# Kernel optimization log

Hardware: AMD Instinct MI355X
Metric: run time of the kernel (lower is better)

Reference implementation:

```python
import jax, jax.numpy as jnp
import numpy as np

NEG = -1e9


def _ln(x, g, b):
    m = x.mean(-1, keepdims=True)
    v = ((x - m) ** 2).mean(-1, keepdims=True)
    return (x - m) / jnp.sqrt(v + 1e-5) * g + b


def _block(single, pair, single_mask, pair_mask,
           pa_ln_g, pa_ln_b, pa_wqkv, pa_wg, pa_wout,
           pt_ln_g, pt_ln_b, pt_w1, pt_b1, pt_w2, pt_b2,
           sa_ln_g, sa_ln_b, sa_wq, sa_wkv, sa_wb, sa_wout,
           st_ln_g, st_ln_b, st_w1, st_b1, st_w2, st_b2):
    B, L, _, D = pair.shape
    H = sa_wb.shape[1]
    hd = D // H
    scale = 1.0 / jnp.sqrt(jnp.asarray(hd, dtype=pair.dtype))
    # ---- PairUpdate: PairAttention over L*L pseudo-tokens ----
    z = _ln(pair, pa_ln_g, pa_ln_b)                       # [B,L,L,D]
    N = L * L
    qkv = (z @ pa_wqkv).reshape(B, N, 3, H, hd)
    q = qkv[:, :, 0].transpose(0, 2, 1, 3)                # [B,H,N,hd]
    k = qkv[:, :, 1].transpose(0, 2, 1, 3)
    v = qkv[:, :, 2].transpose(0, 2, 1, 3)
    attn = jnp.einsum('bhid,bhjd->bhij', q, k) * scale    # [B,H,N,N]
    pm = pair_mask.reshape(B, 1, N)
    m = pm[:, :, :, None] * pm[:, :, None, :]             # [B,1,N,N]
    attn = jnp.where(m > 0, attn, NEG)
    attn = jax.nn.softmax(attn, axis=-1)
    out = jnp.einsum('bhij,bhjd->bhid', attn, v)          # [B,H,N,hd]
    out = out.transpose(0, 2, 1, 3).reshape(B, L, L, D)
    g = jax.nn.sigmoid(z @ pa_wg)
    out = (out @ pa_wout) * g * pair_mask[..., None]
    pair = pair + out
    t = _ln(pair, pt_ln_g, pt_ln_b)
    t = jax.nn.relu(t @ pt_w1 + pt_b1) @ pt_w2 + pt_b2
    pair = pair + t * pair_mask[..., None]
    # ---- SingleUpdate: AttentionPairBias ----
    s = _ln(single, sa_ln_g, sa_ln_b)                     # [B,L,D]
    q = (s @ sa_wq).reshape(B, L, H, hd)
    kv = (s @ sa_wkv).reshape(B, L, 2, H, hd)
    k2, v2 = kv[:, :, 0], kv[:, :, 1]
    attn = jnp.einsum('bihd,bjhd->bhij', q, k2) * scale   # [B,H,L,L]
    bias = (pair @ sa_wb).transpose(0, 3, 1, 2)           # [B,H,L,L]
    attn = attn + bias
    sm = single_mask[:, None, None, :]
    attn = jnp.where(sm > 0, attn, NEG)
    attn = jax.nn.softmax(attn, axis=-1)
    out = jnp.einsum('bhij,bjhd->bihd', attn, v2).reshape(B, L, D)
    single = single + (out @ sa_wout) * single_mask[..., None]
    # single transition
    t = _ln(single, st_ln_g, st_ln_b)
    t = jax.nn.relu(t @ st_w1 + st_b1) @ st_w2 + st_b2
    single = single + t * single_mask[..., None]
    return single, pair


def setup_inputs() -> dict:
    key = jax.random.key(0)
    B, L, D, H = 1, 64, 144, 8
    ks = iter(jax.random.split(key, 40))
    def nrm(shape, scale=0.02):
        return jax.random.normal(next(ks), shape, dtype=jnp.float32) * scale
    sm = jnp.ones((B, L), jnp.float32).at[:, L - 8:].set(0.0)
    pm = sm[:, :, None] * sm[:, None, :]
    return dict(
        single=jax.random.normal(next(ks), (B, L, D), jnp.float32),
        pair=jax.random.normal(next(ks), (B, L, L, D), jnp.float32),
        single_mask=sm,
        pair_mask=pm,
        pa_ln_g=jnp.ones((D,), jnp.float32), pa_ln_b=jnp.zeros((D,), jnp.float32),
        pa_wqkv=nrm((D, 3 * D)), pa_wg=nrm((D, D)), pa_wout=nrm((D, D)),
        pt_ln_g=jnp.ones((D,), jnp.float32), pt_ln_b=jnp.zeros((D,), jnp.float32),
        pt_w1=nrm((D, 4 * D)), pt_b1=jnp.zeros((4 * D,), jnp.float32),
        pt_w2=nrm((4 * D, D)), pt_b2=jnp.zeros((D,), jnp.float32),
        sa_ln_g=jnp.ones((D,), jnp.float32), sa_ln_b=jnp.zeros((D,), jnp.float32),
        sa_wq=nrm((D, D)), sa_wkv=nrm((D, 2 * D)), sa_wb=nrm((D, H)), sa_wout=nrm((D, D)),
        st_ln_g=jnp.ones((D,), jnp.float32), st_ln_b=jnp.zeros((D,), jnp.float32),
        st_w1=nrm((D, 4 * D)), st_b1=jnp.zeros((4 * D,), jnp.float32),
        st_w2=nrm((4 * D, D)), st_b2=jnp.zeros((D,), jnp.float32),
    )


def reference(single, pair, single_mask, pair_mask,
              pa_ln_g, pa_ln_b, pa_wqkv, pa_wg, pa_wout,
              pt_ln_g, pt_ln_b, pt_w1, pt_b1, pt_w2, pt_b2,
              sa_ln_g, sa_ln_b, sa_wq, sa_wkv, sa_wb, sa_wout,
              st_ln_g, st_ln_b, st_w1, st_b1, st_w2, st_b2):
    return _block(single, pair, single_mask, pair_mask,
                  pa_ln_g, pa_ln_b, pa_wqkv, pa_wg, pa_wout,
                  pt_ln_g, pt_ln_b, pt_w1, pt_b1, pt_w2, pt_b2,
                  sa_ln_g, sa_ln_b, sa_wq, sa_wkv, sa_wb, sa_wout,
                  st_ln_g, st_ln_b, st_w1, st_b1, st_w2, st_b2)
```

## Files before the change

kernel.cpp:

```cpp
#include <hip/hip_runtime.h>
#include <hip/hip_bf16.h>

typedef __hip_bfloat16 bf16;
typedef __attribute__((ext_vector_type(8))) short short8;
typedef __attribute__((ext_vector_type(16))) float floatx16;
typedef __attribute__((ext_vector_type(4))) unsigned int uint4v;

__device__ __forceinline__ float tof(bf16 x){ return __bfloat162float(x); }
__device__ __forceinline__ float bflo(unsigned u){ return __uint_as_float(u<<16); }
__device__ __forceinline__ float bfhi(unsigned u){ return __uint_as_float(u & 0xFFFF0000u); }
__device__ __forceinline__ float ldT(const void* p, long i, bool isf){
  return isf ? ((const float*)p)[i] : tof(((const bf16*)p)[i]);
}
__device__ __forceinline__ void stT(void* p, long i, bool isf, float v){
  if (isf) ((float*)p)[i] = v; else ((bf16*)p)[i] = __float2bfloat16(v);
}

#define LL 64
#define DD 144
#define NN 4096
#define HH 8
#define HDIM 18
#define SCALE 0.23570226039551584f
#define LOG2E 1.4426950408889634f

__global__ __launch_bounds__(256) void prep_weights(const unsigned* __restrict__ smaskw,
    int* __restrict__ dflag,
    const void* __restrict__ wqkv, const void* __restrict__ wg,
    const void* __restrict__ wout, const void* __restrict__ w1, const void* __restrict__ w2,
    const void* __restrict__ swq, const void* __restrict__ swkv,
    const void* __restrict__ swout, const void* __restrict__ sw1, const void* __restrict__ sw2,
    bf16* __restrict__ F1, bf16* __restrict__ Fout, bf16* __restrict__ Fw1,
    bf16* __restrict__ Fw2, bf16* __restrict__ Fs1, bf16* __restrict__ Wtswout,
    bf16* __restrict__ Wtst1, bf16* __restrict__ Wtst2){
  bool isf = (smaskw[0] == 0x3F800000u);
  if (blockIdx.x==0 && threadIdx.x==0) dflag[0] = isf ? 4 : 2;
  long t = (long)blockIdx.x*256 + threadIdx.x;
  if (t < 82944){
    int j=t&7, lane=(int)((t>>3)&63); long tk=t>>9; int ks=tk%9, tile=tk/9;
    int col=tile*32+(lane&31); int k=ks*16+(lane>>5)*8+j;
    float v = (col<432)? ldT(wqkv,(long)k*432+col,isf) : ldT(wg,(long)k*144+(col-432),isf);
    F1[t]=__float2bfloat16(v); return;
  } t -= 82944;
  if (t < 23040){
    int j=t&7, lane=(int)((t>>3)&63); long tk=t>>9; int ks=tk%9, tile=tk/9;
    int col=tile*32+(lane&31); if (col>143) col=143;
    int k=ks*16+(lane>>5)*8+j;
    Fout[t]=__float2bfloat16(ldT(wout,(long)k*144+col,isf)); return;
  } t -= 23040;
  if (t < 82944){
    int j=t&7, lane=(int)((t>>3)&63); long tk=t>>9; int ks=tk%9, tile=tk/9;
    int col=tile*32+(lane&31); int k=ks*16+(lane>>5)*8+j;
    Fw1[t]=__float2bfloat16(ldT(w1,(long)k*576+col,isf)); return;
  } t -= 82944;
  if (t < 92160){
    int j=t&7, lane=(int)((t>>3)&63); long tk=t>>9; int ks=tk%36, tile=tk/36;
    int col=tile*32+(lane&31); if (col>143) col=143;
    int k=ks*16+(lane>>5)*8+j;
    Fw2[t]=__float2bfloat16(ldT(w2,(long)k*144+col,isf)); return;
  } t -= 92160;
  if (t < 64512){
    int j=t&7, lane=(int)((t>>3)&63); long tk=t>>9; int ks=tk%9, tile=tk/9;
    int col=tile*32+(lane&31); if (col>431) col=431;
    int k=ks*16+(lane>>5)*8+j;
    float v = (col<144)? ldT(swq,(long)k*144+col,isf) : ldT(swkv,(long)k*288+(col-144),isf);
    Fs1[t]=__float2bfloat16(v); return;
  } t -= 64512;
  if (t < 20736){ int c=t/144,k=t-(long)c*144; Wtswout[t]=__float2bfloat16(ldT(swout,(long)k*144+c,isf)); return; }
  t -= 20736;
  if (t < 82944){ int c=t/144,k=t-(long)c*144; Wtst1[t]=__float2bfloat16(ldT(sw1,(long)k*576+c,isf)); return; }
  t -= 82944;
  if (t < 82944){ int c=t/576,k=t-(long)c*576; Wtst2[t]=__float2bfloat16(ldT(sw2,(long)k*144+c,isf)); return; }
}

__global__ __launch_bounds__(256) void gemm_fused1(const int* __restrict__ df,
    const void* __restrict__ pairv, const void* __restrict__ lng, const void* __restrict__ lnb,
    const bf16* __restrict__ F1,
    const void* __restrict__ pmask,
    bf16* __restrict__ Qb, bf16* __restrict__ Kf, bf16* __restrict__ Vf,
    bf16* __restrict__ gbuf,
    const void* __restrict__ singlev, const void* __restrict__ sag, const void* __restrict__ sab,
    const bf16* __restrict__ Fs1,
    bf16* __restrict__ q_sb, bf16* __restrict__ kv_sb){
  __shared__ short As[64*152];
  bool isf = df[0]==4;
  int tid=threadIdx.x, lane=tid&63, l31=lane&31, w=tid>>6, wr=w>>1, wc=w&1;
  int g=(lane>>5)*8;

  if (blockIdx.y == 64){
    if (blockIdx.x >= 7) return;
    for (int rr=w; rr<64; rr+=4){
      long base=(long)rr*DD;
      float e0=ldT(singlev,base+lane,isf), e1=ldT(singlev,base+lane+64,isf);
      float e2=(lane<16)?ldT(singlev,base+lane+128,isf):0.f;
      float s=e0+e1+e2;
      #pragma unroll
      for (int o=32;o;o>>=1) s += __shfl_xor(s,o);
      float mean=s*(1.f/144.f);
      float d0=e0-mean, d1=e1-mean, d2=(lane<16)?(e2-mean):0.f;
      float v=d0*d0+d1*d1+d2*d2;
      #pragma unroll
      for (int o=32;o;o>>=1) v += __shfl_xor(v,o);
      float rstd=rsqrtf(v*(1.f/144.f)+1e-5f);
      bf16 h0=__float2bfloat16(d0*rstd*ldT(sag,lane,isf)+ldT(sab,lane,isf));
      bf16 h1=__float2bfloat16(d1*rstd*ldT(sag,lane+64,isf)+ldT(sab,lane+64,isf));
      As[rr*152+lane]=*reinterpret_cast<short*>(&h0);
      As[rr*152+lane+64]=*reinterpret_cast<short*>(&h1);
      if (lane<16){
        bf16 h2=__float2bfloat16(d2*rstd*ldT(sag,lane+128,isf)+ldT(sab,lane+128,isf));
        As[rr*152+lane+128]=*reinterpret_cast<short*>(&h2);
      }
    }
    __syncthreads();
    int tile = blockIdx.x*2 + wc;
    const short8* wf = (const short8*)Fs1;
    floatx16 acc;
    #pragma unroll
    for (int i=0;i<16;i++) acc[i]=0.f;
    #pragma unroll
    for (int ks=0; ks<9; ks++){
      short8 af = *(const short8*)&As[(l31+32*wr)*152 + ks*16 + g];
      acc = __builtin_amdgcn_mfma_f32_32x32x16_bf16(af, wf[(tile*9+ks)*64+lane], acc, 0,0,0);
    }
    int col = tile*32 + l31;
    if (col < 432){
      #pragma unroll
      for (int r=0;r<16;r++){
        int row = 32*wr + (r&3)+8*(r>>2)+4*(lane>>5);
        if (col<144) q_sb[(size_t)row*DD+col] = __float2bfloat16(acc[r]);
        else kv_sb[(size_t)row*288+(col-144)] = __float2bfloat16(acc[r]);
      }
    }
    return;
  }

  int row0 = blockIdx.y*64, col0 = blockIdx.x*64;
  for (int rr=w; rr<64; rr+=4){
    long base=(long)(row0+rr)*DD;
    float e0=ldT(pairv,base+lane,isf), e1=ldT(pairv,base+lane+64,isf);
    float e2=(lane<16)?ldT(pairv,base+lane+128,isf):0.f;
    float s=e0+e1+e2;
    #pragma unroll
    for (int o=32;o;o>>=1) s += __shfl_xor(s,o);
    float mean=s*(1.f/144.f);
    float d0=e0-mean, d1=e1-mean, d2=(lane<16)?(e2-mean):0.f;
    float v=d0*d0+d1*d1+d2*d2;
    #pragma unroll
    for (int o=32;o;o>>=1) v += __shfl_xor(v,o);
    float rstd=rsqrtf(v*(1.f/144.f)+1e-5f);
    bf16 h0=__float2bfloat16(d0*rstd*ldT(lng,lane,isf)+ldT(lnb,lane,isf));
    bf16 h1=__float2bfloat16(d1*rstd*ldT(lng,lane+64,isf)+ldT(lnb,lane+64,isf));
    As[rr*152+lane]=*reinterpret_cast<short*>(&h0);
    As[rr*152+lane+64]=*reinterpret_cast<short*>(&h1);
    if (lane<16){
      bf16 h2=__float2bfloat16(d2*rstd*ldT(lng,lane+128,isf)+ldT(lnb,lane+128,isf));
      As[rr*152+lane+128]=*reinterpret_cast<short*>(&h2);
    }
  }
  __syncthreads();
  int tile = blockIdx.x*2 + wc;
  const short8* wf = (const short8*)F1;
  floatx16 acc;
  #pragma unroll
  for (int i=0;i<16;i++) acc[i]=0.f;
  #pragma unroll
  for (int ks=0; ks<9; ks++){
    short8 af = *(const short8*)&As[(l31+32*wr)*152 + ks*16 + g];
    acc = __builtin_amdgcn_mfma_f32_32x32x16_bf16(af, wf[(tile*9+ks)*64+lane], acc, 0,0,0);
  }
  int col = col0 + wc*32 + l31;
  #pragma unroll
  for (int r=0;r<16;r++){
    int row = row0 + 32*wr + (r&3)+8*(r>>2)+4*(lane>>5);
    if (col < 144){
      int hh = col/18, d = col - hh*18;
      Qb[((size_t)hh*NN+row)*32 + d] = __float2bfloat16(acc[r]*(SCALE*LOG2E));
    } else if (col < 288){
      int c2 = col-144, hh = c2/18, d = c2 - hh*18;
      int f = d>>4, rem = d&15, gs = rem>>3, j = rem&7;
      Kf[((((size_t)hh*128 + (row>>5))*2 + f)*64 + gs*32 + (row&31))*8 + j]
        = __float2bfloat16(acc[r]);
    } else if (col < 432){
      int c2 = col-288, hh = c2/18, d = c2 - hh*18;
      float pm = (ldT(pmask,row,isf)>0.f)?1.f:0.f;
      int kin = row&31, f = kin>>4, k15 = kin&15;
      int gs = (k15>>2)&1, j = (k15&3) | (((k15>>3)&1)<<2);
      Vf[((((size_t)hh*128 + (row>>5))*2 + f)*64 + gs*32 + d)*8 + j]
        = __float2bfloat16(acc[r]*pm);
    } else {
      int c2 = col-432;
      float gt = 1.f/(1.f+__expf(fminf(-acc[r],30.f)));
      gbuf[(size_t)row*DD+c2] = __float2bfloat16(gt);
    }
  }
  if (blockIdx.x==0){
    for (int t=threadIdx.x; t<64*8*7; t+=256){
      int n = row0 + t/56; int rem = t%56; int hh = rem/7, dw = rem%7 + 9;
      ((unsigned*)(Qb + ((size_t)hh*NN+n)*32))[dw] = 0;
    }
    for (int t=threadIdx.x; t<64*8; t+=256){
      int n = row0 + (t>>3), hh = t&7;
      float pm = (ldT(pmask,n,isf)>0.f)?1.f:0.f;
      int kin = n&31, f = kin>>4, k15 = kin&15;
      int gs = (k15>>2)&1, j = (k15&3) | (((k15>>3)&1)<<2);
      Vf[((((size_t)hh*128 + (n>>5))*2 + f)*64 + gs*32 + 18)*8 + j] = __float2bfloat16(pm);
    }
  }
}

__global__ __launch_bounds__(256) void pair_attn_mfma(const int* __restrict__ df,
    const bf16* __restrict__ Qb, const bf16* __restrict__ Kf,
    const bf16* __restrict__ Vf, bf16* __restrict__ aob){
  __shared__ float Comb[4][32][20];
  int h = blockIdx.x & 7, qt = blockIdx.x >> 3;
  int tid = threadIdx.x;
  int w = tid >> 6, lane = tid & 63;
  int l31 = lane & 31, gsel = lane>>5;

  const unsigned* qp = (const unsigned*)(Qb + ((size_t)h*NN + qt*32 + l31)*32);
  short8 qf0, qf1;
  #pragma unroll
  for (int j=0;j<4;j++) ((unsigned*)&qf0)[j] = qp[gsel*4+j];
  #pragma unroll
  for (int j=0;j<4;j++) ((unsigned*)&qf1)[j] = qp[8+gsel*4+j];

  floatx16 o;
  #pragma unroll
  for (int i=0;i<16;i++) o[i]=0.f;

  const short8* kf8 = (const short8*)Kf + (size_t)h*16384;
  const short8* vf8 = (const short8*)Vf + (size_t)h*16384;
  int c0 = w*32;

  short8 af0 = kf8[(c0*2+0)*64 + lane];
  short8 af1 = kf8[(c0*2+1)*64 + lane];
  short8 av0 = vf8[(c0*2+0)*64 + lane];
  short8 av1 = vf8[(c0*2+1)*64 + lane];

  for (int cc=0; cc<32; cc++){
    int cn = c0 + (cc<31 ? cc+1 : 31);
    short8 naf0 = kf8[(cn*2+0)*64 + lane];
    short8 naf1 = kf8[(cn*2+1)*64 + lane];
    short8 nav0 = vf8[(cn*2+0)*64 + lane];
    short8 nav1 = vf8[(cn*2+1)*64 + lane];

    floatx16 s;
    #pragma unroll
    for (int i=0;i<16;i++) s[i]=0.f;
    __builtin_amdgcn_s_setprio(1);
    s = __builtin_amdgcn_mfma_f32_32x32x16_bf16(af0, qf0, s, 0,0,0);
    s = __builtin_amdgcn_mfma_f32_32x32x16_bf16(af1, qf1, s, 0,0,0);
    __builtin_amdgcn_s_setprio(0);

    short8 P1, P2;
    #pragma unroll
    for (int j=0;j<4;j++){
      unsigned e0 = __float_as_uint(__builtin_amdgcn_exp2f(s[2*j]));
      unsigned e1 = __float_as_uint(__builtin_amdgcn_exp2f(s[2*j+1]));
      ((unsigned*)&P1)[j] = (e0>>16) | (e1 & 0xFFFF0000u);
      unsigned e2 = __float_as_uint(__builtin_amdgcn_exp2f(s[8+2*j]));
      unsigned e3 = __float_as_uint(__builtin_amdgcn_exp2f(s[9+2*j]));
      ((unsigned*)&P2)[j] = (e2>>16) | (e3 & 0xFFFF0000u);
    }

    __builtin_amdgcn_s_setprio(1);
    o = __builtin_amdgcn_mfma_f32_32x32x16_bf16(av0, P1, o, 0,0,0);
    o = __builtin_amdgcn_mfma_f32_32x32x16_bf16(av1, P2, o, 0,0,0);
    __builtin_amdgcn_s_setprio(0);

    af0=naf0; af1=naf1; av0=nav0; av1=nav1;
  }

  #pragma unroll
  for (int r=0;r<16;r++){
    int d = (r&3) + 8*(r>>2) + 4*gsel;
    if (d < 20) Comb[w][l31][d] = o[r];
  }
  __syncthreads();
  for (int t=tid; t<32*HDIM; t+=256){
    int q = t/HDIM, d = t-q*HDIM;
    float num = Comb[0][q][d]+Comb[1][q][d]+Comb[2][q][d]+Comb[3][q][d];
    float den = Comb[0][q][18]+Comb[1][q][18]+Comb[2][q][18]+Comb[3][q][18];
    aob[(size_t)(qt*32+q)*DD + h*HDIM + d] = __float2bfloat16(num/fmaxf(den,1e-20f));
  }
}

__global__ __launch_bounds__(512) void pair_tail(const int* __restrict__ df,
    const bf16* __restrict__ aob, const bf16* __restrict__ gbuf,
    const void* __restrict__ pairv, const void* __restrict__ pmaskv,
    const bf16* __restrict__ Fout, const void* __restrict__ ptln_g, const void* __restrict__ ptln_b,
    const bf16* __restrict__ Fw1, const void* __restrict__ b1v,
    const bf16* __restrict__ Fw2, const void* __restrict__ b2v,
    const void* __restrict__ wb, void* __restrict__ outP, long outOff,
    float* __restrict__ biasb){
  __shared__ __align__(16) char smem[65536];
  float* p1  = (float*)smem;
  short* ts  = (short*)(smem + 18432);
  short* hh_ = (short*)(smem + 28160);
  float* outv = (float*)(smem + 28160);

  bool isf = df[0]==4;
  int tid=threadIdx.x, lane=tid&63, l31=lane&31, gsel=lane>>5, g=gsel*8;
  int w=tid>>6;
  int r0 = blockIdx.x*32;
  const short8* foutf = (const short8*)Fout;
  const short8* fw1f  = (const short8*)Fw1;
  const short8* fw2f  = (const short8*)Fw2;

  for (int t=tid; t<32*72; t+=512){
    int m=t/72, dw=t%72;
    ((unsigned*)ts)[m*76+dw] = ((const unsigned*)(aob + (size_t)(r0+m)*144))[dw];
  }
  __syncthreads();

  for (int tile=w; tile<5; tile+=8){
    int c0=tile*32;
    floatx16 acc;
    #pragma unroll
    for (int i=0;i<16;i++) acc[i]=0.f;
    #pragma unroll
    for (int ks=0; ks<9; ks++){
      short8 af = *(const short8*)&ts[l31*152 + ks*16 + g];
      acc = __builtin_amdgcn_mfma_f32_32x32x16_bf16(af, foutf[(tile*9+ks)*64+lane], acc, 0,0,0);
    }
    if (c0+l31 < 144){
      #pragma unroll
      for (int r=0;r<16;r++){
        int row=(r&3)+8*(r>>2)+4*gsel;
        p1[row*144 + c0+l31] = acc[r];
      }
    }
  }
  __syncthreads();
  for (int t=tid; t<32*144; t+=512){
    int row=t/144; int col=t-row*144;
    long gidx=(long)(r0+row)*144 + col;
    float pm = (ldT(pmaskv, r0+row, isf)>0.f)?1.f:0.f;
    p1[t] = ldT(pairv,gidx,isf) + p1[t]*tof(gbuf[gidx])*pm;
  }
  __syncthreads();
  for (int rr=w; rr<32; rr+=8){
    float e0=p1[rr*144+lane], e1=p1[rr*144+lane+64], e2=(lane<16)?p1[rr*144+lane+128]:0.f;
    float s=e0+e1+e2;
    #pragma unroll
    for (int o=32;o;o>>=1) s += __shfl_xor(s,o);
    float mean=s*(1.f/144.f);
    float d0=e0-mean, d1=e1-mean, d2=(lane<16)?(e2-mean):0.f;
    float v=d0*d0+d1*d1+d2*d2;
    #pragma unroll
    for (int o=32;o;o>>=1) v += __shfl_xor(v,o);
    float rstd=rsqrtf(v*(1.f/144.f)+1e-5f);
    bf16 h0 = __float2bfloat16(d0*rstd*ldT(ptln_g,lane,isf)    + ldT(ptln_b,lane,isf));
    bf16 h1 = __float2bfloat16(d1*rstd*ldT(ptln_g,lane+64,isf) + ldT(ptln_b,lane+64,isf));
    ts[rr*152+lane]    = *reinterpret_cast<short*>(&h0);
    ts[rr*152+lane+64] = *reinterpret_cast<short*>(&h1);
    if (lane<16){
      bf16 h2 = __float2bfloat16(d2*rstd*ldT(ptln_g,lane+128,isf) + ldT(ptln_b,lane+128,isf));
      ts[rr*152+lane+128] = *reinterpret_cast<short*>(&h2);
    }
  }
  __syncthreads();
  for (int tile=w; tile<18; tile+=8){
    int c0=tile*32, colB=c0+l31;
    floatx16 acc;
    #pragma unroll
    for (int i=0;i<16;i++) acc[i]=0.f;
    #pragma unroll
    for (int ks=0; ks<9; ks++){
      short8 af = *(const short8*)&ts[l31*152 + ks*16 + g];
      acc = __builtin_amdgcn_mfma_f32_32x32x16_bf16(af, fw1f[(tile*9+ks)*64+lane], acc, 0,0,0);
    }
    float bb = ldT(b1v,colB,isf);
    #pragma unroll
    for (int r=0;r<16;r++){
      int row=(r&3)+8*(r>>2)+4*gsel;
      bf16 hv = __float2bfloat16(fmaxf(acc[r]+bb,0.f));
      hh_[row*584 + colB] = *reinterpret_cast<short*>(&hv);
    }
  }
  __syncthreads();
  floatx16 fin; int fc0 = -1;
  for (int tile=w; tile<5; tile+=8){
    int c0=tile*32;
    int colB=c0+l31; if (colB>143) colB=143;
    floatx16 acc;
    #pragma unroll
    for (int i=0;i<16;i++) acc[i]=0.f;
    #pragma unroll
    for (int ks=0; ks<36; ks++){
      short8 af = *(const short8*)&hh_[l31*584 + ks*16 + g];
      acc = __builtin_amdgcn_mfma_f32_32x32x16_bf16(af, fw2f[(tile*36+ks)*64+lane], acc, 0,0,0);
    }
    float bb = ldT(b2v,colB,isf);
    #pragma unroll
    for (int r=0;r<16;r++){
      int row=(r&3)+8*(r>>2)+4*gsel;
      float pm = (ldT(pmaskv, r0+row, isf)>0.f)?1.f:0.f;
      float val = p1[row*144 + colB] + (acc[r]+bb)*pm;
      if (c0+l31 < 144)
        stT(outP, outOff + (long)(r0+row)*144 + c0+l31, isf, val);
      fin[r]=val;
    }
    fc0 = c0;
  }
  __syncthreads();
  if (fc0 >= 0 && fc0+l31 < 144){
    #pragma unroll
    for (int r=0;r<16;r++){
      int row=(r&3)+8*(r>>2)+4*gsel;
      outv[row*144 + fc0+l31] = fin[r];
    }
  }
  __syncthreads();
  if (tid < 256){
    int n = tid>>3, hb = tid&7;
    float acc=0.f;
    #pragma unroll 4
    for (int k=0;k<144;k++) acc += outv[n*144+k]*ldT(wb,k*8+hb,isf);
    biasb[(size_t)(r0+n)*8+hb]=acc;
  }
}

__global__ __launch_bounds__(256) void single_tail(const int* __restrict__ df,
    const void* __restrict__ single, const bf16* __restrict__ q_sb,
    const bf16* __restrict__ kv_sb, const float* __restrict__ biasb,
    const void* __restrict__ smask, const bf16* __restrict__ Wtswout,
    const void* __restrict__ stln_g, const void* __restrict__ stln_b,
    const bf16* __restrict__ Wtst1, const void* __restrict__ st_b1,
    const bf16* __restrict__ Wtst2, const void* __restrict__ st_b2,
    void* __restrict__ outS){
  bool isf = df[0]==4;
  __shared__ __align__(16) short kvs[64*288];
  __shared__ float pexp[8][64];
  __shared__ float tot[8];
  __shared__ __align__(16) float bb[512];
  __shared__ float qs[DD], as_[DD], s1[DD], tss[DD], hs[576];
  __shared__ float mr[2];
  int n = blockIdx.x, tid = threadIdx.x;
  {
    const uint4v* src = (const uint4v*)kv_sb;
    uint4v* dst = (uint4v*)kvs;
    for (int t=tid; t<2304; t+=256) dst[t] = src[t];
  }
  if (tid<DD) qs[tid] = tof(q_sb[(size_t)n*DD+tid]);
  {
    const uint4v* src = (const uint4v*)(biasb + (size_t)n*512);
    uint4v* dst = (uint4v*)bb;
    if (tid<128) dst[tid] = src[tid];
  }
  __syncthreads();
  #pragma unroll
  for (int pp=0; pp<2; pp++){
    int pi = tid + pp*256;
    int h = pi>>6, j = pi&63;
    const unsigned* kr = (const unsigned*)&kvs[j*288 + h*HDIM];
    float s=0.f;
    #pragma unroll
    for (int i=0;i<9;i++){
      unsigned u = kr[i];
      s += qs[h*HDIM+2*i]*bflo(u) + qs[h*HDIM+2*i+1]*bfhi(u);
    }
    s = fminf(s*SCALE + bb[j*8+h], 30.f);
    pexp[h][j] = (ldT(smask,j,isf)>0.f) ? __expf(s) : 0.f;
  }
  __syncthreads();
  if (tid<64){
    int h=tid>>3, j0=(tid&7)*8;
    float t2=0.f;
    #pragma unroll
    for (int j=0;j<8;j++) t2 += pexp[h][j0+j];
    #pragma unroll
    for (int o=4;o;o>>=1) t2 += __shfl_xor(t2,o);
    if ((tid&7)==0) tot[h] = fmaxf(t2,1e-20f);
  }
  __syncthreads();
  if (tid<DD){
    int h = tid/HDIM;
    float a0=0.f, a1=0.f;
    #pragma unroll 8
    for (int j=0;j<64;j+=2){
      unsigned u0 = ((unsigned)(unsigned short)kvs[j*288 + 144 + tid])<<16;
      unsigned u1 = ((unsigned)(unsigned short)kvs[(j+1)*288 + 144 + tid])<<16;
      a0 += pexp[h][j]*__uint_as_float(u0);
      a1 += pexp[h][j+1]*__uint_as_float(u1);
    }
    as_[tid] = (a0+a1)/tot[h];
  }
  __syncthreads();
  float sm = ldT(smask,n,isf);
  if (tid<DD){
    const uint4v* wr = (const uint4v*)(Wtswout + (size_t)tid*DD);
    float a0=0.f, a1=0.f;
    #pragma unroll 3
    for (int kw=0; kw<18; kw+=2){
      uint4v u = wr[kw], u2 = wr[kw+1];
      a0 += as_[8*kw+0]*bflo(u[0]) + as_[8*kw+1]*bfhi(u[0])
          + as_[8*kw+2]*bflo(u[1]) + as_[8*kw+3]*bfhi(u[1])
          + as_[8*kw+4]*bflo(u[2]) + as_[8*kw+5]*bfhi(u[2])
          + as_[8*kw+6]*bflo(u[3]) + as_[8*kw+7]*bfhi(u[3]);
      a1 += as_[8*kw+8]*bflo(u2[0]) + as_[8*kw+9]*bfhi(u2[0])
          + as_[8*kw+10]*bflo(u2[1]) + as_[8*kw+11]*bfhi(u2[1])
          + as_[8*kw+12]*bflo(u2[2]) + as_[8*kw+13]*bfhi(u2[2])
          + as_[8*kw+14]*bflo(u2[3]) + as_[8*kw+15]*bfhi(u2[3]);
    }
    s1[tid] = ldT(single,(long)n*DD+tid,isf) + (a0+a1)*sm;
  }
  __syncthreads();
  if (tid < 64){
    float e0 = s1[tid], e1 = s1[tid+64], e2 = (tid<16)?s1[tid+128]:0.f;
    float s = e0+e1+e2;
    #pragma unroll
    for (int o=32;o;o>>=1) s += __shfl_xor(s,o);
    float mean = s*(1.f/144.f);
    float d0=e0-mean, d1=e1-mean, d2=(tid<16)?(e2-mean):0.f;
    float v = d0*d0+d1*d1+d2*d2;
    #pragma unroll
    for (int o=32;o;o>>=1) v += __shfl_xor(v,o);
    if (tid==0){ mr[0]=mean; mr[1]=rsqrtf(v*(1.f/144.f)+1e-5f); }
  }
  __syncthreads();
  if (tid<DD) tss[tid] = (s1[tid]-mr[0])*mr[1]*ldT(stln_g,tid,isf) + ldT(stln_b,tid,isf);
  __syncthreads();
  for (int c=tid;c<576;c+=256){
    const uint4v* wr = (const uint4v*)(Wtst1 + (size_t)c*DD);
    float a0=ldT(st_b1,c,isf), a1=0.f;
    #pragma unroll 3
    for (int kw=0; kw<18; kw+=2){
      uint4v u = wr[kw], u2 = wr[kw+1];
      a0 += tss[8*kw+0]*bflo(u[0]) + tss[8*kw+1]*bfhi(u[0])
          + tss[8*kw+2]*bflo(u[1]) + tss[8*kw+3]*bfhi(u[1])
          + tss[8*kw+4]*bflo(u[2]) + tss[8*kw+5]*bfhi(u[2])
          + tss[8*kw+6]*bflo(u[3]) + tss[8*kw+7]*bfhi(u[3]);
      a1 += tss[8*kw+8]*bflo(u2[0]) + tss[8*kw+9]*bfhi(u2[0])
          + tss[8*kw+10]*bflo(u2[1]) + tss[8*kw+11]*bfhi(u2[1])
          + tss[8*kw+12]*bflo(u2[2]) + tss[8*kw+13]*bfhi(u2[2])
          + tss[8*kw+14]*bflo(u2[3]) + tss[8*kw+15]*bfhi(u2[3]);
    }
    hs[c]=fmaxf(a0+a1,0.f);
  }
  __syncthreads();
  if (tid<DD){
    const uint4v* wr = (const uint4v*)(Wtst2 + (size_t)tid*576);
    float a0=ldT(st_b2,tid,isf), a1=0.f;
    #pragma unroll 4
    for (int kw=0; kw<72; kw+=2){
      uint4v u = wr[kw], u2 = wr[kw+1];
      a0 += hs[8*kw+0]*bflo(u[0]) + hs[8*kw+1]*bfhi(u[0])
          + hs[8*kw+2]*bflo(u[1]) + hs[8*kw+3]*bfhi(u[1])
          + hs[8*kw+4]*bflo(u[2]) + hs[8*kw+5]*bfhi(u[2])
          + hs[8*kw+6]*bflo(u[3]) + hs[8*kw+7]*bfhi(u[3]);
      a1 += hs[8*kw+8]*bflo(u2[0]) + hs[8*kw+9]*bfhi(u2[0])
          + hs[8*kw+10]*bflo(u2[1]) + hs[8*kw+11]*bfhi(u2[1])
          + hs[8*kw+12]*bflo(u2[2]) + hs[8*kw+13]*bfhi(u2[2])
          + hs[8*kw+14]*bflo(u2[3]) + hs[8*kw+15]*bfhi(u2[3]);
    }
    stT(outS,(long)n*DD+tid,isf, s1[tid] + (a0+a1)*sm);
  }
}

extern "C" void kernel_launch(void* const* d_in, const int* in_sizes, int n_in,
                              void* d_out, int out_size, void* d_ws, size_t ws_size,
                              hipStream_t stream) {
  char* wsb = (char*)d_ws;
  int*   dflag = (int*)wsb;
  bf16*  F1     = (bf16*)(wsb + 16);
  bf16*  Fout   = F1 + 82944;
  bf16*  Fw1    = Fout + 23040;
  bf16*  Fw2    = Fw1 + 82944;
  bf16*  Fs1    = Fw2 + 92160;
  bf16*  Wtswout= Fs1 + 64512;
  bf16*  Wtst1  = Wtswout + 20736;
  bf16*  Wtst2  = Wtst1 + 82944;
  bf16*  Qb   = Wtst2 + 82944;
  bf16*  Kf   = Qb + (size_t)HH*NN*32;
  bf16*  Vf   = Kf + (size_t)HH*131072;
  bf16*  gbuf = Vf + (size_t)HH*131072;
  bf16*  aob  = gbuf + (size_t)NN*DD;
  float* biasb= (float*)(aob + (size_t)NN*DD);
  bf16*  q_sb = (bf16*)(biasb + NN*8);
  bf16*  kv_sb= q_sb + LL*DD;

  const long OUTP_OFF = (long)LL*DD;

  prep_weights<<<2079,256,0,stream>>>((const unsigned*)d_in[2], dflag,
      d_in[6], d_in[7], d_in[8], d_in[11], d_in[13],
      d_in[17], d_in[18], d_in[20], d_in[23], d_in[25],
      F1, Fout, Fw1, Fw2, Fs1, Wtswout, Wtst1, Wtst2);

  gemm_fused1<<<dim3(9,65),256,0,stream>>>(dflag, d_in[1], d_in[4], d_in[5], F1, d_in[3],
                                           Qb, Kf, Vf, gbuf,
                                           d_in[0], d_in[15], d_in[16], Fs1, q_sb, kv_sb);
  pair_attn_mfma<<<1024,256,0,stream>>>(dflag, Qb, Kf, Vf, aob);
  pair_tail<<<128,512,0,stream>>>(dflag, aob, gbuf, d_in[1], d_in[3],
                                  Fout, d_in[9], d_in[10], Fw1, d_in[12],
                                  Fw2, d_in[14], d_in[19], d_out, OUTP_OFF, biasb);
  single_tail<<<LL,256,0,stream>>>(dflag, d_in[0], q_sb, kv_sb, biasb, d_in[2],
                                   Wtswout, d_in[21], d_in[22], Wtst1, d_in[24],
                                   Wtst2, d_in[26], d_out);
  (void)in_sizes; (void)n_in; (void)out_size; (void)ws_size;
}
```

Baseline: 225.2 us.

## Process two query tiles per attention block and split single_tail reductions across 512 threads

The pair attention kernel now computes two 32-row query tiles per block. Each loaded K/V fragment is reused for both, which halves K/V global traffic per query, and the grid drops from 1024 to 512 blocks. The cost is more registers for the second accumulator and Q fragments, plus fewer blocks to fill the GPU. Separately, single_tail moves to 512 threads and splits its attention-value, output-projection and FFN2 dot products into segments, reduced through a shared partial buffer, to shorten the serial per-thread loops at the price of extra barriers.

```diff
diff --git a/kernel.cpp b/kernel.cpp
--- a/kernel.cpp
+++ b/kernel.cpp
@@ -212,21 +212,26 @@
     const bf16* __restrict__ Qb, const bf16* __restrict__ Kf,
     const bf16* __restrict__ Vf, bf16* __restrict__ aob){
   __shared__ float Comb[4][32][20];
-  int h = blockIdx.x & 7, qt = blockIdx.x >> 3;
+  int h = blockIdx.x & 7, qp2 = blockIdx.x >> 3;
+  int qtA = qp2*2, qtB = qp2*2+1;
   int tid = threadIdx.x;
   int w = tid >> 6, lane = tid & 63;
   int l31 = lane & 31, gsel = lane>>5;
 
-  const unsigned* qp = (const unsigned*)(Qb + ((size_t)h*NN + qt*32 + l31)*32);
-  short8 qf0, qf1;
+  const unsigned* qpA = (const unsigned*)(Qb + ((size_t)h*NN + qtA*32 + l31)*32);
+  const unsigned* qpB = (const unsigned*)(Qb + ((size_t)h*NN + qtB*32 + l31)*32);
+  short8 qa0, qa1, qb0, qb1;
   #pragma unroll
-  for (int j=0;j<4;j++) ((unsigned*)&qf0)[j] = qp[gsel*4+j];
+  for (int j=0;j<4;j++){
+    ((unsigned*)&qa0)[j] = qpA[gsel*4+j];
+    ((unsigned*)&qa1)[j] = qpA[8+gsel*4+j];
+    ((unsigned*)&qb0)[j] = qpB[gsel*4+j];
+    ((unsigned*)&qb1)[j] = qpB[8+gsel*4+j];
+  }
+
+  floatx16 oA, oB;
   #pragma unroll
-  for (int j=0;j<4;j++) ((unsigned*)&qf1)[j] = qp[8+gsel*4+j];
-
-  floatx16 o;
-  #pragma unroll
-  for (int i=0;i<16;i++) o[i]=0.f;
+  for (int i=0;i<16;i++){ oA[i]=0.f; oB[i]=0.f; }
 
   const short8* kf8 = (const short8*)Kf + (size_t)h*16384;
   const short8* vf8 = (const short8*)Vf + (size_t)h*16384;
@@ -245,14 +250,13 @@
     short8 nav1 = vf8[(cn*2+1)*64 + lane];
 
     floatx16 s;
+    short8 P1, P2;
     #pragma unroll
     for (int i=0;i<16;i++) s[i]=0.f;
     __builtin_amdgcn_s_setprio(1);
-    s = __builtin_amdgcn_mfma_f32_32x32x16_bf16(af0, qf0, s, 0,0,0);
-    s = __builtin_amdgcn_mfma_f32_32x32x16_bf16(af1, qf1, s, 0,0,0);
+    s = __builtin_amdgcn_mfma_f32_32x32x16_bf16(af0, qa0, s, 0,0,0);
+    s = __builtin_amdgcn_mfma_f32_32x32x16_bf16(af1, qa1, s, 0,0,0);
     __builtin_amdgcn_s_setprio(0);
-
-    short8 P1, P2;
     #pragma unroll
     for (int j=0;j<4;j++){
       unsigned e0 = __float_as_uint(__builtin_amdgcn_exp2f(s[2*j]));
@@ -262,10 +266,28 @@
       unsigned e3 = __float_as_uint(__builtin_amdgcn_exp2f(s[9+2*j]));
       ((unsigned*)&P2)[j] = (e2>>16) | (e3 & 0xFFFF0000u);
     }
-
     __builtin_amdgcn_s_setprio(1);
-    o = __builtin_amdgcn_mfma_f32_32x32x16_bf16(av0, P1, o, 0,0,0);
-    o = __builtin_amdgcn_mfma_f32_32x32x16_bf16(av1, P2, o, 0,0,0);
+    oA = __builtin_amdgcn_mfma_f32_32x32x16_bf16(av0, P1, oA, 0,0,0);
+    oA = __builtin_amdgcn_mfma_f32_32x32x16_bf16(av1, P2, oA, 0,0,0);
+    __builtin_amdgcn_s_setprio(0);
+    #pragma unroll
+    for (int i=0;i<16;i++) s[i]=0.f;
+    __builtin_amdgcn_s_setprio(1);
+    s = __builtin_amdgcn_mfma_f32_32x32x16_bf16(af0, qb0, s, 0,0,0);
+    s = __builtin_amdgcn_mfma_f32_32x32x16_bf16(af1, qb1, s, 0,0,0);
+    __builtin_amdgcn_s_setprio(0);
+    #pragma unroll
+    for (int j=0;j<4;j++){
+      unsigned e0 = __float_as_uint(__builtin_amdgcn_exp2f(s[2*j]));
+      unsigned e1 = __float_as_uint(__builtin_amdgcn_exp2f(s[2*j+1]));
+      ((unsigned*)&P1)[j] = (e0>>16) | (e1 & 0xFFFF0000u);
+      unsigned e2 = __float_as_uint(__builtin_amdgcn_exp2f(s[8+2*j]));
+      unsigned e3 = __float_as_uint(__builtin_amdgcn_exp2f(s[9+2*j]));
+      ((unsigned*)&P2)[j] = (e2>>16) | (e3 & 0xFFFF0000u);
+    }
+    __builtin_amdgcn_s_setprio(1);
+    oB = __builtin_amdgcn_mfma_f32_32x32x16_bf16(av0, P1, oB, 0,0,0);
+    oB = __builtin_amdgcn_mfma_f32_32x32x16_bf16(av1, P2, oB, 0,0,0);
     __builtin_amdgcn_s_setprio(0);
 
     af0=naf0; af1=naf1; av0=nav0; av1=nav1;
@@ -274,14 +296,27 @@
   #pragma unroll
   for (int r=0;r<16;r++){
     int d = (r&3) + 8*(r>>2) + 4*gsel;
-    if (d < 20) Comb[w][l31][d] = o[r];
+    if (d < 20) Comb[w][l31][d] = oA[r];
   }
   __syncthreads();
   for (int t=tid; t<32*HDIM; t+=256){
     int q = t/HDIM, d = t-q*HDIM;
     float num = Comb[0][q][d]+Comb[1][q][d]+Comb[2][q][d]+Comb[3][q][d];
     float den = Comb[0][q][18]+Comb[1][q][18]+Comb[2][q][18]+Comb[3][q][18];
-    aob[(size_t)(qt*32+q)*DD + h*HDIM + d] = __float2bfloat16(num/fmaxf(den,1e-20f));
+    aob[(size_t)(qtA*32+q)*DD + h*HDIM + d] = __float2bfloat16(num/fmaxf(den,1e-20f));
+  }
+  __syncthreads();
+  #pragma unroll
+  for (int r=0;r<16;r++){
+    int d = (r&3) + 8*(r>>2) + 4*gsel;
+    if (d < 20) Comb[w][l31][d] = oB[r];
+  }
+  __syncthreads();
+  for (int t=tid; t<32*HDIM; t+=256){
+    int q = t/HDIM, d = t-q*HDIM;
+    float num = Comb[0][q][d]+Comb[1][q][d]+Comb[2][q][d]+Comb[3][q][d];
+    float den = Comb[0][q][18]+Comb[1][q][18]+Comb[2][q][18]+Comb[3][q][18];
+    aob[(size_t)(qtB*32+q)*DD + h*HDIM + d] = __float2bfloat16(num/fmaxf(den,1e-20f));
   }
 }
 
@@ -421,7 +456,7 @@
   }
 }
 
-__global__ __launch_bounds__(256) void single_tail(const int* __restrict__ df,
+__global__ __launch_bounds__(512) void single_tail(const int* __restrict__ df,
     const void* __restrict__ single, const bf16* __restrict__ q_sb,
     const bf16* __restrict__ kv_sb, const float* __restrict__ biasb,
     const void* __restrict__ smask, const bf16* __restrict__ Wtswout,
@@ -431,16 +466,17 @@
     void* __restrict__ outS){
   bool isf = df[0]==4;
   __shared__ __align__(16) short kvs[64*288];
-  __shared__ float pexp[8][64];
+  __shared__ float pexp[512];
   __shared__ float tot[8];
   __shared__ __align__(16) float bb[512];
-  __shared__ float qs[DD], as_[DD], s1[DD], tss[DD], hs[576];
+  __shared__ float part[576];
+  __shared__ float qs[DD], as_[DD], s1v[DD], tss[DD], hs[576];
   __shared__ float mr[2];
   int n = blockIdx.x, tid = threadIdx.x;
   {
     const uint4v* src = (const uint4v*)kv_sb;
     uint4v* dst = (uint4v*)kvs;
-    for (int t=tid; t<2304; t+=256) dst[t] = src[t];
+    for (int t=tid; t<2304; t+=512) dst[t] = src[t];
   }
   if (tid<DD) qs[tid] = tof(q_sb[(size_t)n*DD+tid]);
   {
@@ -449,10 +485,8 @@
     if (tid<128) dst[tid] = src[tid];
   }
   __syncthreads();
-  #pragma unroll
-  for (int pp=0; pp<2; pp++){
-    int pi = tid + pp*256;
-    int h = pi>>6, j = pi&63;
+  {
+    int h = tid>>6, j = tid&63;
     const unsigned* kr = (const unsigned*)&kvs[j*288 + h*HDIM];
     float s=0.f;
     #pragma unroll
@@ -461,53 +495,58 @@
       s += qs[h*HDIM+2*i]*bflo(u) + qs[h*HDIM+2*i+1]*bfhi(u);
     }
     s = fminf(s*SCALE + bb[j*8+h], 30.f);
-    pexp[h][j] = (ldT(smask,j,isf)>0.f) ? __expf(s) : 0.f;
+    pexp[tid] = (ldT(smask,j,isf)>0.f) ? __expf(s) : 0.f;
   }
   __syncthreads();
   if (tid<64){
     int h=tid>>3, j0=(tid&7)*8;
     float t2=0.f;
     #pragma unroll
-    for (int j=0;j<8;j++) t2 += pexp[h][j0+j];
+    for (int j=0;j<8;j++) t2 += pexp[h*64+j0+j];
     #pragma unroll
     for (int o=4;o;o>>=1) t2 += __shfl_xor(t2,o);
     if ((tid&7)==0) tot[h] = fmaxf(t2,1e-20f);
   }
   __syncthreads();
+  for (int t=tid; t<576; t+=512){
+    int seg=t/144, d=t-seg*144, h=d/HDIM, j0=seg*16;
+    float a0=0.f, a1=0.f;
+    #pragma unroll
+    for (int j=0;j<16;j+=2){
+      unsigned u0 = ((unsigned)(unsigned short)kvs[(j0+j)*288 + 144 + d])<<16;
+      unsigned u1 = ((unsigned)(unsigned short)kvs[(j0+j+1)*288 + 144 + d])<<16;
+      a0 += pexp[h*64+j0+j]*__uint_as_float(u0);
+      a1 += pexp[h*64+j0+j+1]*__uint_as_float(u1);
+    }
+    part[seg*144+d]=a0+a1;
+  }
+  __syncthreads();
   if (tid<DD){
     int h = tid/HDIM;
-    float a0=0.f, a1=0.f;
-    #pragma unroll 8
-    for (int j=0;j<64;j+=2){
-      unsigned u0 = ((unsigned)(unsigned short)kvs[j*288 + 144 + tid])<<16;
-      unsigned u1 = ((unsigned)(unsigned short)kvs[(j+1)*288 + 144 + tid])<<16;
-      a0 += pexp[h][j]*__uint_as_float(u0);
-      a1 += pexp[h][j+1]*__uint_as_float(u1);
-    }
-    as_[tid] = (a0+a1)/tot[h];
+    as_[tid] = (part[tid]+part[144+tid]+part[288+tid]+part[432+tid])/tot[h];
   }
   __syncthreads();
   float sm = ldT(smask,n,isf);
-  if (tid<DD){
-    const uint4v* wr = (const uint4v*)(Wtswout + (size_t)tid*DD);
-    float a0=0.f, a1=0.f;
-    #pragma unroll 3
-    for (int kw=0; kw<18; kw+=2){
-      uint4v u = wr[kw], u2 = wr[kw+1];
-      a0 += as_[8*kw+0]*bflo(u[0]) + as_[8*kw+1]*bfhi(u[0])
-          + as_[8*kw+2]*bflo(u[1]) + as_[8*kw+3]*bfhi(u[1])
-          + as_[8*kw+4]*bflo(u[2]) + as_[8*kw+5]*bfhi(u[2])
-          + as_[8*kw+6]*bflo(u[3]) + as_[8*kw+7]*bfhi(u[3]);
-      a1 += as_[8*kw+8]*bflo(u2[0]) + as_[8*kw+9]*bfhi(u2[0])
-          + as_[8*kw+10]*bflo(u2[1]) + as_[8*kw+11]*bfhi(u2[1])
-          + as_[8*kw+12]*bflo(u2[2]) + as_[8*kw+13]*bfhi(u2[2])
-          + as_[8*kw+14]*bflo(u2[3]) + as_[8*kw+15]*bfhi(u2[3]);
-    }
-    s1[tid] = ldT(single,(long)n*DD+tid,isf) + (a0+a1)*sm;
-  }
+  if (tid<288){
+    int seg=tid/144, d=tid-seg*144;
+    const uint4v* wr = (const uint4v*)(Wtswout + (size_t)d*DD) + seg*9;
+    int b0=seg*72;
+    float a=0.f;
+    #pragma unroll
+    for (int kw=0; kw<9; kw++){
+      uint4v u = wr[kw]; int e=b0+8*kw;
+      a += as_[e]*bflo(u[0]) + as_[e+1]*bfhi(u[0])
+         + as_[e+2]*bflo(u[1]) + as_[e+3]*bfhi(u[1])
+         + as_[e+4]*bflo(u[2]) + as_[e+5]*bfhi(u[2])
+         + as_[e+6]*bflo(u[3]) + as_[e+7]*bfhi(u[3]);
+    }
+    part[seg*144+d]=a;
+  }
+  __syncthreads();
+  if (tid<DD) s1v[tid] = ldT(single,(long)n*DD+tid,isf) + (part[tid]+part[144+tid])*sm;
   __syncthreads();
   if (tid < 64){
-    float e0 = s1[tid], e1 = s1[tid+64], e2 = (tid<16)?s1[tid+128]:0.f;
+    float e0 = s1v[tid], e1 = s1v[tid+64], e2 = (tid<16)?s1v[tid+128]:0.f;
     float s = e0+e1+e2;
     #pragma unroll
     for (int o=32;o;o>>=1) s += __shfl_xor(s,o);
@@ -519,9 +558,9 @@
     if (tid==0){ mr[0]=mean; mr[1]=rsqrtf(v*(1.f/144.f)+1e-5f); }
   }
   __syncthreads();
-  if (tid<DD) tss[tid] = (s1[tid]-mr[0])*mr[1]*ldT(stln_g,tid,isf) + ldT(stln_b,tid,isf);
-  __syncthreads();
-  for (int c=tid;c<576;c+=256){
+  if (tid<DD) tss[tid] = (s1v[tid]-mr[0])*mr[1]*ldT(stln_g,tid,isf) + ldT(stln_b,tid,isf);
+  __syncthreads();
+  for (int c=tid; c<576; c+=512){
     const uint4v* wr = (const uint4v*)(Wtst1 + (size_t)c*DD);
     float a0=ldT(st_b1,c,isf), a1=0.f;
     #pragma unroll 3
@@ -539,23 +578,30 @@
     hs[c]=fmaxf(a0+a1,0.f);
   }
   __syncthreads();
-  if (tid<DD){
-    const uint4v* wr = (const uint4v*)(Wtst2 + (size_t)tid*576);
-    float a0=ldT(st_b2,tid,isf), a1=0.f;
-    #pragma unroll 4
-    for (int kw=0; kw<72; kw+=2){
+  for (int t=tid; t<576; t+=512){
+    int seg=t/144, d=t-seg*144;
+    const uint4v* wr = (const uint4v*)(Wtst2 + (size_t)d*576) + seg*18;
+    int b0=seg*144;
+    float a0=0.f, a1=0.f;
+    #pragma unroll 3
+    for (int kw=0; kw<18; kw+=2){
       uint4v u = wr[kw], u2 = wr[kw+1];
-      a0 += hs[8*kw+0]*bflo(u[0]) + hs[8*kw+1]*bfhi(u[0])
-          + hs[8*kw+2]*bflo(u[1]) + hs[8*kw+3]*bfhi(u[1])
-          + hs[8*kw+4]*bflo(u[2]) + hs[8*kw+5]*bfhi(u[2])
-          + hs[8*kw+6]*bflo(u[3]) + hs[8*kw+7]*bfhi(u[3]);
-      a1 += hs[8*kw+8]*bflo(u2[0]) + hs[8*kw+9]*bfhi(u2[0])
-          + hs[8*kw+10]*bflo(u2[1]) + hs[8*kw+11]*bfhi(u2[1])
-          + hs[8*kw+12]*bflo(u2[2]) + hs[8*kw+13]*bfhi(u2[2])
-          + hs[8*kw+14]*bflo(u2[3]) + hs[8*kw+15]*bfhi(u2[3]);
-    }
-    stT(outS,(long)n*DD+tid,isf, s1[tid] + (a0+a1)*sm);
-  }
+      int e=b0+8*kw;
+      a0 += hs[e]*bflo(u[0]) + hs[e+1]*bfhi(u[0])
+          + hs[e+2]*bflo(u[1]) + hs[e+3]*bfhi(u[1])
+          + hs[e+4]*bflo(u[2]) + hs[e+5]*bfhi(u[2])
+          + hs[e+6]*bflo(u[3]) + hs[e+7]*bfhi(u[3]);
+      a1 += hs[e+8]*bflo(u2[0]) + hs[e+9]*bfhi(u2[0])
+          + hs[e+10]*bflo(u2[1]) + hs[e+11]*bfhi(u2[1])
+          + hs[e+12]*bflo(u2[2]) + hs[e+13]*bfhi(u2[2])
+          + hs[e+14]*bflo(u2[3]) + hs[e+15]*bfhi(u2[3]);
+    }
+    part[seg*144+d]=a0+a1;
+  }
+  __syncthreads();
+  if (tid<DD)
+    stT(outS,(long)n*DD+tid,isf,
+        s1v[tid] + (ldT(st_b2,tid,isf)+part[tid]+part[144+tid]+part[288+tid]+part[432+tid])*sm);
 }
 
 extern "C" void kernel_launch(void* const* d_in, const int* in_sizes, int n_in,
@@ -590,11 +636,11 @@
   gemm_fused1<<<dim3(9,65),256,0,stream>>>(dflag, d_in[1], d_in[4], d_in[5], F1, d_in[3],
                                            Qb, Kf, Vf, gbuf,
                                            d_in[0], d_in[15], d_in[16], Fs1, q_sb, kv_sb);
-  pair_attn_mfma<<<1024,256,0,stream>>>(dflag, Qb, Kf, Vf, aob);
+  pair_attn_mfma<<<512,256,0,stream>>>(dflag, Qb, Kf, Vf, aob);
   pair_tail<<<128,512,0,stream>>>(dflag, aob, gbuf, d_in[1], d_in[3],
                                   Fout, d_in[9], d_in[10], Fw1, d_in[12],
                                   Fw2, d_in[14], d_in[19], d_out, OUTP_OFF, biasb);
-  single_tail<<<LL,256,0,stream>>>(dflag, d_in[0], q_sb, kv_sb, biasb, d_in[2],
+  single_tail<<<LL,512,0,stream>>>(dflag, d_in[0], q_sb, kv_sb, biasb, d_in[2],
                                    Wtswout, d_in[21], d_in[22], Wtst1, d_in[24],
                                    Wtst2, d_in[26], d_out);
   (void)in_sizes; (void)n_in; (void)out_size; (void)ws_size;
```

Measured after the change: 217.9 us. -3.3%, faster.
